# Kernel tuning notes

Hardware: AMD Instinct MI355X
Metric: run time of the kernel (lower is better)

## Reference

```python
import jax, jax.numpy as jnp
import numpy as np

EMB = 1024
HEADS = 16
HEADSIZE = EMB // HEADS
LN_EPS = 1e-5


def layernorm(x, w, b):
    # normalize over last dim (headsize)
    mu = jnp.mean(x, axis=-1, keepdims=True)
    var = jnp.var(x, axis=-1, keepdims=True)
    return (x - mu) * jax.lax.rsqrt(var + LN_EPS) * w + b


def setup_inputs() -> dict:
    key = jax.random.key(0)
    ks = jax.random.split(key, 8)
    B, S, C = 2, 2048, 2048
    x = jax.random.normal(ks[0], (B, S, EMB), dtype=jnp.float32)
    context = jax.random.normal(ks[1], (B, C, EMB), dtype=jnp.float32)
    mask = jnp.ones((B, S), dtype=jnp.float32)
    contextMask = jnp.ones((B, C), dtype=jnp.float32)
    s = 0.02
    Wq = jax.random.normal(ks[2], (EMB, EMB), dtype=jnp.float32) * s
    Wk = jax.random.normal(ks[3], (EMB, EMB), dtype=jnp.float32) * s
    Wv = jax.random.normal(ks[4], (EMB, EMB), dtype=jnp.float32) * s
    Wu = jax.random.normal(ks[5], (EMB, EMB), dtype=jnp.float32) * s
    bu = jnp.zeros((EMB,), dtype=jnp.float32)
    qln_w = jnp.ones((HEADSIZE,), dtype=jnp.float32)
    qln_b = jnp.zeros((HEADSIZE,), dtype=jnp.float32)
    kln_w = jnp.ones((HEADSIZE,), dtype=jnp.float32)
    kln_b = jnp.zeros((HEADSIZE,), dtype=jnp.float32)
    return {"x": x, "context": context, "mask": mask, "contextMask": contextMask,
            "Wq": Wq, "Wk": Wk, "Wv": Wv, "Wu": Wu, "bu": bu,
            "qln_w": qln_w, "qln_b": qln_b, "kln_w": kln_w, "kln_b": kln_b}


def reference(x, context, mask, contextMask, Wq, Wk, Wv, Wu, bu, qln_w, qln_b, kln_w, kln_b):
    B, S, E = x.shape
    C = context.shape[1]
    T = S + C
    xc = jnp.concatenate([x, context], axis=1)            # [B, T, E]
    q = (x @ Wq).reshape(B, S, HEADS, HEADSIZE)
    k = (xc @ Wk).reshape(B, T, HEADS, HEADSIZE)
    v = (xc @ Wv).reshape(B, T, HEADS, HEADSIZE)
    q = layernorm(q, qln_w, qln_b)
    k = layernorm(k, kln_w, kln_b)
    scale = E ** 0.25
    q = q / scale
    k = k / scale
    # [B, H, S, T] score matrix (explicitly materialized, as in the original)
    dot = jnp.einsum('bshd,bthd->bhst', q, k)
    mcat = jnp.concatenate([mask, contextMask], axis=1)   # [B, T]
    dotMask = mask[:, None, :, None] * mcat[:, None, None, :]  # [B,1,S,T]
    # hand-rolled masked softmax: softmax(dot*mask) * mask, renormalize
    p = jax.nn.softmax(dot * dotMask, axis=-1) * dotMask
    p = p / (jnp.sum(p, axis=-1, keepdims=True) + 1e-13)
    out = jnp.einsum('bhst,bthd->bshd', p, v).reshape(B, S, E)
    return out @ Wu + bu
```

## Files before the change

kernel.cpp:

```cpp
#include <hip/hip_runtime.h>
#include <hip/hip_bf16.h>
#include <cstdint>

#define B_SZ   2
#define S_LEN  2048
#define C_LEN  2048
#define T_LEN  4096
#define EMB_   1024
#define HEADS_ 16
#define D_     64

typedef __attribute__((ext_vector_type(8))) short bf16x8;
typedef __attribute__((ext_vector_type(4))) float f32x4;
typedef __attribute__((ext_vector_type(16))) float f32x16;
typedef __attribute__((ext_vector_type(2))) float f32x2;

__device__ __forceinline__ unsigned short f2bf(float f) {
    unsigned u = __builtin_bit_cast(unsigned, f);
    u += 0x7fffu + ((u >> 16) & 1u);
    return (unsigned short)(u >> 16);
}
__device__ __forceinline__ float bf2f(unsigned short h) {
    return __builtin_bit_cast(float, (unsigned)h << 16);
}

__global__ void build_xcb_k(const float* __restrict__ x, const float* __restrict__ ctx,
                            unsigned short* __restrict__ xcb) {
    int i = blockIdx.x * blockDim.x + threadIdx.x;
    size_t e8 = (size_t)i * 8;
    int b = (int)(e8 / ((size_t)T_LEN * EMB_));
    size_t rem = e8 % ((size_t)T_LEN * EMB_);
    int t = (int)(rem / EMB_);
    int c = (int)(rem % EMB_);
    const float* src = (t < S_LEN)
        ? &x[((size_t)b * S_LEN + t) * EMB_ + c]
        : &ctx[((size_t)b * C_LEN + (t - S_LEN)) * EMB_ + c];
    float4 v0 = ((const float4*)src)[0];
    float4 v1 = ((const float4*)src)[1];
    uint4 o;
    o.x = (unsigned)f2bf(v0.x) | ((unsigned)f2bf(v0.y) << 16);
    o.y = (unsigned)f2bf(v0.z) | ((unsigned)f2bf(v0.w) << 16);
    o.z = (unsigned)f2bf(v1.x) | ((unsigned)f2bf(v1.y) << 16);
    o.w = (unsigned)f2bf(v1.z) | ((unsigned)f2bf(v1.w) << 16);
    *(uint4*)&xcb[e8] = o;
}

__global__ void mcat_k(const float* __restrict__ mask, const float* __restrict__ cmask,
                       float* __restrict__ Mcat) {
    int i = blockIdx.x * 256 + threadIdx.x;
    int b = i / T_LEN, t = i % T_LEN;
    Mcat[i] = (t < S_LEN) ? mask[(size_t)b * S_LEN + t]
                          : cmask[(size_t)b * C_LEN + (t - S_LEN)];
}

__global__ void wtrans4_k(const float* __restrict__ W0, const float* __restrict__ W1,
                          const float* __restrict__ W2, const float* __restrict__ W3,
                          unsigned short* __restrict__ T0, unsigned short* __restrict__ T1,
                          unsigned short* __restrict__ T2, unsigned short* __restrict__ T3) {
    __shared__ __align__(16) unsigned short tile[64][72];
    int bx = blockIdx.x, by = blockIdx.y, bz = blockIdx.z;
    const float* W = (bz == 0) ? W0 : (bz == 1) ? W1 : (bz == 2) ? W2 : W3;
    unsigned short* WT = (bz == 0) ? T0 : (bz == 1) ? T1 : (bz == 2) ? T2 : T3;
    int tid = threadIdx.x;
#pragma unroll
    for (int r = 0; r < 4; ++r) {
        int idx = tid + r * 256;
        int row = idx >> 4, c4 = idx & 15;
        float4 v = ((const float4*)&W[((size_t)(by * 64 + row)) * EMB_ + bx * 64])[c4];
        tile[row][c4 * 4 + 0] = f2bf(v.x);
        tile[row][c4 * 4 + 1] = f2bf(v.y);
        tile[row][c4 * 4 + 2] = f2bf(v.z);
        tile[row][c4 * 4 + 3] = f2bf(v.w);
    }
    __syncthreads();
#pragma unroll
    for (int r = 0; r < 2; ++r) {
        int idx = tid + r * 256;
        int n = idx >> 3, k8 = idx & 7;
        uint4 o;
        unsigned q[4];
#pragma unroll
        for (int j = 0; j < 4; ++j)
            q[j] = (unsigned)tile[k8 * 8 + 2 * j][n] | ((unsigned)tile[k8 * 8 + 2 * j + 1][n] << 16);
        o.x = q[0]; o.y = q[1]; o.z = q[2]; o.w = q[3];
        *(uint4*)&WT[((size_t)(bx * 64 + n)) * EMB_ + by * 64 + k8 * 8] = o;
    }
}

__global__ __launch_bounds__(256) void gemm_qkv_k(
    const unsigned short* __restrict__ A,
    const unsigned short* __restrict__ Bt,
    unsigned short* __restrict__ Yk,
    unsigned short* __restrict__ Yv,
    unsigned short* __restrict__ Yq) {
    constexpr int KTOT = 1024, NTOT = 1024;
    int nt = blockIdx.x, mt = blockIdx.y;
    if (nt >= 16 && (mt & 31) >= 16) return;
    __shared__ __align__(16) unsigned short As[128 * 32];
    __shared__ __align__(16) unsigned short Bs[128 * 32];
    int in_row0 = mt * 128;
    unsigned short* Cout;
    int col0, out_row0;
    if (nt < 8)       { Cout = Yk; col0 = nt * 128;        out_row0 = mt * 128; }
    else if (nt < 16) { Cout = Yv; col0 = (nt - 8) * 128;  out_row0 = mt * 128; }
    else              { Cout = Yq; col0 = (nt - 16) * 128;
                        out_row0 = (mt >> 5) * 2048 + (mt & 31) * 128; }
    int tid = threadIdx.x, w = tid >> 6, l = tid & 63, l15 = l & 15, lg = l >> 4;
    int wr = (w >> 1) * 64, wc = (w & 1) * 64;

    f32x4 zero4 = {0.f, 0.f, 0.f, 0.f};
    f32x4 acc[4][4];
#pragma unroll
    for (int i = 0; i < 4; ++i)
#pragma unroll
        for (int j = 0; j < 4; ++j) acc[i][j] = zero4;

    for (int k0 = 0; k0 < KTOT; k0 += 32) {
#pragma unroll
        for (int j = 0; j < 2; ++j) {
            int o = tid * 16 + j * 4096;
            int row = o >> 6;
            int ke = (o & 63) >> 1;
            __builtin_amdgcn_global_load_lds(
                (const __attribute__((address_space(1))) void*)&A[(size_t)(in_row0 + row) * KTOT + k0 + ke],
                (__attribute__((address_space(3))) void*)&As[o >> 1], 16, 0, 0);
            __builtin_amdgcn_global_load_lds(
                (const __attribute__((address_space(1))) void*)&Bt[(size_t)(nt * 128 + row) * KTOT + k0 + ke],
                (__attribute__((address_space(3))) void*)&Bs[o >> 1], 16, 0, 0);
        }
        __syncthreads();
        bf16x8 af[4], bf[4];
#pragma unroll
        for (int fr = 0; fr < 4; ++fr)
            af[fr] = *(const bf16x8*)&As[(wr + fr * 16 + l15) * 32 + lg * 8];
#pragma unroll
        for (int fc = 0; fc < 4; ++fc)
            bf[fc] = *(const bf16x8*)&Bs[(wc + fc * 16 + l15) * 32 + lg * 8];
#pragma unroll
        for (int fr = 0; fr < 4; ++fr)
#pragma unroll
            for (int fc = 0; fc < 4; ++fc)
                acc[fr][fc] = __builtin_amdgcn_mfma_f32_16x16x32_bf16(af[fr], bf[fc], acc[fr][fc], 0, 0, 0);
        __syncthreads();
    }
#pragma unroll
    for (int fr = 0; fr < 4; ++fr) {
#pragma unroll
        for (int fc = 0; fc < 4; ++fc) {
            int row = out_row0 + wr + fr * 16 + lg * 4;
            int col = col0 + wc + fc * 16 + l15;
#pragma unroll
            for (int i = 0; i < 4; ++i)
                Cout[(size_t)(row + i) * NTOT + col] = f2bf(acc[fr][fc][i]);
        }
    }
}

template <bool F32OUT>
__global__ __launch_bounds__(256) void gemm_bt_k(
    const unsigned short* __restrict__ A,
    const unsigned short* __restrict__ Bt,
    void* __restrict__ Cout,
    const float* __restrict__ bias,
    int mtiles_per_chunk, int chunk_stride) {
    constexpr int KTOT = 1024, NTOT = 1024;
    __shared__ __align__(16) unsigned short As[128 * 32];
    __shared__ __align__(16) unsigned short Bs[128 * 32];
    int nt = blockIdx.x, mt = blockIdx.y;
    int in_row0 = (mt / mtiles_per_chunk) * chunk_stride + (mt % mtiles_per_chunk) * 128;
    int out_row0 = mt * 128;
    int tid = threadIdx.x, w = tid >> 6, l = tid & 63, l15 = l & 15, lg = l >> 4;
    int wr = (w >> 1) * 64, wc = (w & 1) * 64;

    f32x4 zero4 = {0.f, 0.f, 0.f, 0.f};
    f32x4 acc[4][4];
#pragma unroll
    for (int i = 0; i < 4; ++i)
#pragma unroll
        for (int j = 0; j < 4; ++j) acc[i][j] = zero4;

    for (int k0 = 0; k0 < KTOT; k0 += 32) {
#pragma unroll
        for (int j = 0; j < 2; ++j) {
            int o = tid * 16 + j * 4096;
            int row = o >> 6;
            int ke = (o & 63) >> 1;
            __builtin_amdgcn_global_load_lds(
                (const __attribute__((address_space(1))) void*)&A[(size_t)(in_row0 + row) * KTOT + k0 + ke],
                (__attribute__((address_space(3))) void*)&As[o >> 1], 16, 0, 0);
            __builtin_amdgcn_global_load_lds(
                (const __attribute__((address_space(1))) void*)&Bt[(size_t)(nt * 128 + row) * KTOT + k0 + ke],
                (__attribute__((address_space(3))) void*)&Bs[o >> 1], 16, 0, 0);
        }
        __syncthreads();
        bf16x8 af[4], bf[4];
#pragma unroll
        for (int fr = 0; fr < 4; ++fr)
            af[fr] = *(const bf16x8*)&As[(wr + fr * 16 + l15) * 32 + lg * 8];
#pragma unroll
        for (int fc = 0; fc < 4; ++fc)
            bf[fc] = *(const bf16x8*)&Bs[(wc + fc * 16 + l15) * 32 + lg * 8];
#pragma unroll
        for (int fr = 0; fr < 4; ++fr)
#pragma unroll
            for (int fc = 0; fc < 4; ++fc)
                acc[fr][fc] = __builtin_amdgcn_mfma_f32_16x16x32_bf16(af[fr], bf[fc], acc[fr][fc], 0, 0, 0);
        __syncthreads();
    }
#pragma unroll
    for (int fr = 0; fr < 4; ++fr) {
#pragma unroll
        for (int fc = 0; fc < 4; ++fc) {
            int row = out_row0 + wr + fr * 16 + lg * 4;
            int col = nt * 128 + wc + fc * 16 + l15;
#pragma unroll
            for (int i = 0; i < 4; ++i) {
                float v = acc[fr][fc][i];
                if (F32OUT) {
                    ((float*)Cout)[(size_t)(row + i) * NTOT + col] = v + bias[col];
                } else {
                    ((unsigned short*)Cout)[(size_t)(row + i) * NTOT + col] = f2bf(v);
                }
            }
        }
    }
}

__global__ void ln_head_k(const unsigned short* __restrict__ Y,
                          unsigned short* __restrict__ Out,
                          const float* __restrict__ lw, const float* __restrict__ lb,
                          const float* __restrict__ Mcat,
                          int rows_per_b, float scale) {
    int gw = blockIdx.x * 4 + (threadIdx.x >> 6);
    int lane = threadIdx.x & 63;
    int h = gw % HEADS_;
    int row = gw / HEADS_;
    int b = row / rows_per_b, r = row % rows_per_b;
    float v = bf2f(Y[(size_t)row * EMB_ + h * 64 + lane]);
    float s = v, s2 = v * v;
#pragma unroll
    for (int m = 1; m <= 32; m <<= 1) {
        s += __shfl_xor(s, m);
        s2 += __shfl_xor(s2, m);
    }
    float mu = s * (1.f / 64.f);
    float var = s2 * (1.f / 64.f) - mu * mu;
    float o = (v - mu) * rsqrtf(var + 1e-5f) * lw[lane] + lb[lane];
    float mq = Mcat[(size_t)b * T_LEN + r];
    Out[(((size_t)b * HEADS_ + h) * rows_per_b + r) * 64 + lane] = f2bf(o * scale * mq);
}

__global__ void ln_head_pack_k(const unsigned short* __restrict__ Y,
                               unsigned short* __restrict__ KF,
                               const float* __restrict__ lw, const float* __restrict__ lb,
                               const float* __restrict__ Mcat,
                               float scale) {
    int gw = blockIdx.x * 4 + (threadIdx.x >> 6);
    int lane = threadIdx.x & 63;
    int h = gw % HEADS_;
    int row = gw / HEADS_;
    int b = row / T_LEN, r = row % T_LEN;
    float v = bf2f(Y[(size_t)row * EMB_ + h * 64 + lane]);
    float s = v, s2 = v * v;
#pragma unroll
    for (int m = 1; m <= 32; m <<= 1) {
        s += __shfl_xor(s, m);
        s2 += __shfl_xor(s2, m);
    }
    float mu = s * (1.f / 64.f);
    float var = s2 * (1.f / 64.f) - mu * mu;
    float o = (v - mu) * rsqrtf(var + 1e-5f) * lw[lane] + lb[lane];
    float mt = Mcat[(size_t)b * T_LEN + r];
    int bh = b * HEADS_ + h;
    int kt = r >> 5, l31 = r & 31;
    int sf = lane >> 4, hi = (lane >> 3) & 1, j = lane & 7;
    size_t flat = ((((size_t)bh * 128 + kt) * 4 + sf) * 64 + hi * 32 + l31) * 8 + j;
    KF[flat] = f2bf(o * scale * mt);
}

__global__ void vpack_k(const unsigned short* __restrict__ Yv, unsigned short* __restrict__ VF,
                        const float* __restrict__ Mcat) {
    __shared__ __align__(16) unsigned short tile[64][72];
    __shared__ float msk[64];
    int t0 = blockIdx.x * 64;
    int bh = blockIdx.y;
    int b = bh >> 4, h = bh & 15;
    int tid = threadIdx.x;
    if (tid < 64) msk[tid] = Mcat[(size_t)b * T_LEN + t0 + tid];
#pragma unroll
    for (int rr = 0; rr < 2; ++rr) {
        int idx = tid + rr * 256;
        int row = idx >> 3, c8 = idx & 7;
        *(uint4*)&tile[row][c8 * 8] =
            *(const uint4*)&Yv[((size_t)b * T_LEN + t0 + row) * EMB_ + h * 64 + c8 * 8];
    }
    __syncthreads();
    int f = tid >> 6, l = tid & 63;
    int d = (f >> 1) * 32 + (l & 31);
    int tb = (f & 1) * 16 + 4 * (l >> 5);
#pragma unroll
    for (int ktl = 0; ktl < 2; ++ktl) {
        unsigned short e[8];
#pragma unroll
        for (int j = 0; j < 8; ++j) {
            int tt = ktl * 32 + tb + (j >> 2) * 8 + (j & 3);
            e[j] = f2bf(bf2f(tile[tt][d]) * msk[tt]);
        }
        uint4 o;
        o.x = (unsigned)e[0] | ((unsigned)e[1] << 16);
        o.y = (unsigned)e[2] | ((unsigned)e[3] << 16);
        o.z = (unsigned)e[4] | ((unsigned)e[5] << 16);
        o.w = (unsigned)e[6] | ((unsigned)e[7] << 16);
        size_t kt = (size_t)blockIdx.x * 2 + ktl;
        *(uint4*)&VF[((((size_t)bh * 128 + kt) * 4 + f) * 64 + l) * 8] = o;
    }
}

#define SOFTMAX(SA, MT, LS, PB0, PB1) do {                                        \
    f32x2 e2[8];                                                                  \
    _Pragma("unroll") for (int i_ = 0; i_ < 8; ++i_) {                            \
        e2[i_][0] = __builtin_amdgcn_exp2f(SA[2 * i_]);                           \
        e2[i_][1] = __builtin_amdgcn_exp2f(SA[2 * i_ + 1]);                       \
    }                                                                             \
    {                                                                             \
        float rsA_ = 0.f, rsB_ = 0.f;                                             \
        _Pragma("unroll") for (int i_ = 0; i_ < 8; ++i_) {                        \
            rsA_ = fmaf(e2[i_][0], MT[2 * i_], rsA_);                             \
            rsB_ = fmaf(e2[i_][1], MT[2 * i_ + 1], rsB_);                         \
        }                                                                         \
        float rs_ = rsA_ + rsB_;                                                  \
        rs_ += __shfl_xor(rs_, 32);                                               \
        (LS) += rs_;                                                              \
    }                                                                             \
    unsigned pk_[8];                                                              \
    _Pragma("unroll") for (int d_ = 0; d_ < 8; ++d_)                              \
        asm("v_cvt_pk_bf16_f32 %0, %1, %2" : "=v"(pk_[d_])                        \
            : "v"(e2[d_][0]), "v"(e2[d_][1]));                                    \
    { uint4 u0_; u0_.x=pk_[0]; u0_.y=pk_[1]; u0_.z=pk_[2]; u0_.w=pk_[3];          \
      uint4 u1_; u1_.x=pk_[4]; u1_.y=pk_[5]; u1_.z=pk_[6]; u1_.w=pk_[7];          \
      (PB0) = __builtin_bit_cast(bf16x8, u0_);                                    \
      (PB1) = __builtin_bit_cast(bf16x8, u1_); }                                  \
} while (0)

__global__ __launch_bounds__(256) void attn32_k(
    const unsigned short* __restrict__ Q,
    const unsigned short* __restrict__ KF,
    const unsigned short* __restrict__ VF,
    const float* __restrict__ Mcat,
    unsigned short* __restrict__ O) {
    __shared__ __align__(16) unsigned short Ks[4][2048];
    __shared__ __align__(16) unsigned short Vs[4][2048];
    __shared__ float OldsF[4][64][32];
    __shared__ float Llds[4][32];

    int bid = blockIdx.x;
    int xcd = bid & 7, slot = bid >> 3;
    int bh = xcd * 4 + (slot >> 4);
    int qblk = slot & 15;
    int b = bh >> 4, h = bh & 15;
    int tid = threadIdx.x;
    int w = tid >> 6;
    int lane = tid & 63;
    int l31 = lane & 31;
    int hi = lane >> 5;
    int q0 = qblk * 128;
    int qw = q0 + w * 32;

    const unsigned short* KFb_ = KF + (size_t)bh * 262144;
    const unsigned short* VFb_ = VF + (size_t)bh * 262144;
    const float* Mb = Mcat + (size_t)b * T_LEN;

    bf16x8 qf[4];
    {
        const unsigned short* Qp = Q + ((size_t)bh * S_LEN + qw + l31) * 64 + hi * 8;
#pragma unroll
        for (int s = 0; s < 4; ++s) qf[s] = *(const bf16x8*)(Qp + s * 16);
    }

    f32x16 Z16;
#pragma unroll
    for (int i = 0; i < 16; ++i) Z16[i] = 0.f;
    f32x16 acc0 = Z16, acc1 = Z16;
    float lS = 0.f;

#define STAGE(BUF, KT) do {                                                        \
    __builtin_amdgcn_global_load_lds(                                              \
        (const __attribute__((address_space(1))) void*)(KFb_ + (size_t)(KT) * 2048 + tid * 8), \
        (__attribute__((address_space(3))) void*)&Ks[BUF][tid * 8], 16, 0, 0);     \
    __builtin_amdgcn_global_load_lds(                                              \
        (const __attribute__((address_space(1))) void*)(VFb_ + (size_t)(KT) * 2048 + tid * 8), \
        (__attribute__((address_space(3))) void*)&Vs[BUF][tid * 8], 16, 0, 0);     \
} while (0)

    STAGE(0, 0); STAGE(1, 1);
    __syncthreads();

    for (int it = 0; it < 64; ++it) {
        int base = (it & 1) << 1;
        int kt0 = it * 2;
        if (it < 63) {
            STAGE(base ^ 2, kt0 + 2);
            STAGE((base ^ 2) + 1, kt0 + 3);
        }
        const float* mb0 = Mb + kt0 * 32 + 4 * hi;
        float4 am0 = *(const float4*)(mb0);
        float4 am1 = *(const float4*)(mb0 + 8);
        float4 am2 = *(const float4*)(mb0 + 16);
        float4 am3 = *(const float4*)(mb0 + 24);
        float4 bm0 = *(const float4*)(mb0 + 32);
        float4 bm1 = *(const float4*)(mb0 + 40);
        float4 bm2 = *(const float4*)(mb0 + 48);
        float4 bm3 = *(const float4*)(mb0 + 56);
        bf16x8 kfrA[4], vfrA[4], kfrB[4], vfrB[4];
#pragma unroll
        for (int s = 0; s < 4; ++s) {
            kfrA[s] = *(const bf16x8*)&Ks[base][s * 512 + lane * 8];
            vfrA[s] = *(const bf16x8*)&Vs[base][s * 512 + lane * 8];
            kfrB[s] = *(const bf16x8*)&Ks[base + 1][s * 512 + lane * 8];
            vfrB[s] = *(const bf16x8*)&Vs[base + 1][s * 512 + lane * 8];
        }
        f32x16 saA = Z16, saB = Z16;
#pragma unroll
        for (int s = 0; s < 4; ++s) {
            saA = __builtin_amdgcn_mfma_f32_32x32x16_bf16(kfrA[s], qf[s], saA, 0, 0, 0);
            saB = __builtin_amdgcn_mfma_f32_32x32x16_bf16(kfrB[s], qf[s], saB, 0, 0, 0);
        }
        float mtA_[16], mtB_[16];
        mtA_[0] = am0.x; mtA_[1] = am0.y; mtA_[2]  = am0.z; mtA_[3]  = am0.w;
        mtA_[4] = am1.x; mtA_[5] = am1.y; mtA_[6]  = am1.z; mtA_[7]  = am1.w;
        mtA_[8] = am2.x; mtA_[9] = am2.y; mtA_[10] = am2.z; mtA_[11] = am2.w;
        mtA_[12] = am3.x; mtA_[13] = am3.y; mtA_[14] = am3.z; mtA_[15] = am3.w;
        mtB_[0] = bm0.x; mtB_[1] = bm0.y; mtB_[2]  = bm0.z; mtB_[3]  = bm0.w;
        mtB_[4] = bm1.x; mtB_[5] = bm1.y; mtB_[6]  = bm1.z; mtB_[7]  = bm1.w;
        mtB_[8] = bm2.x; mtB_[9] = bm2.y; mtB_[10] = bm2.z; mtB_[11] = bm2.w;
        mtB_[12] = bm3.x; mtB_[13] = bm3.y; mtB_[14] = bm3.z; mtB_[15] = bm3.w;
        bf16x8 p0A, p1A, p0B, p1B;
        SOFTMAX(saA, mtA_, lS, p0A, p1A);
        SOFTMAX(saB, mtB_, lS, p0B, p1B);
        acc0 = __builtin_amdgcn_mfma_f32_32x32x16_bf16(vfrA[0], p0A, acc0, 0, 0, 0);
        acc1 = __builtin_amdgcn_mfma_f32_32x32x16_bf16(vfrA[2], p0A, acc1, 0, 0, 0);
        acc0 = __builtin_amdgcn_mfma_f32_32x32x16_bf16(vfrA[1], p1A, acc0, 0, 0, 0);
        acc1 = __builtin_amdgcn_mfma_f32_32x32x16_bf16(vfrA[3], p1A, acc1, 0, 0, 0);
        acc0 = __builtin_amdgcn_mfma_f32_32x32x16_bf16(vfrB[0], p0B, acc0, 0, 0, 0);
        acc1 = __builtin_amdgcn_mfma_f32_32x32x16_bf16(vfrB[2], p0B, acc1, 0, 0, 0);
        acc0 = __builtin_amdgcn_mfma_f32_32x32x16_bf16(vfrB[1], p1B, acc0, 0, 0, 0);
        acc1 = __builtin_amdgcn_mfma_f32_32x32x16_bf16(vfrB[3], p1B, acc1, 0, 0, 0);
        __syncthreads();
    }
#undef STAGE

#pragma unroll
    for (int r = 0; r < 16; ++r) {
        int dl = (r & 3) + 8 * (r >> 2) + 4 * hi;
        OldsF[w][dl][l31] = acc0[r];
        OldsF[w][dl + 32][l31] = acc1[r];
    }
    if (hi == 0) Llds[w][l31] = lS;
    __syncthreads();
    {
        int rr = lane >> 1, hf = lane & 1;
        float L = Llds[w][rr];
        float invL = 1.f / (L + 1e-13f);
        float mqz = Mb[q0 + w * 32 + rr];
        invL = (mqz != 0.f) ? invL : 0.f;
        float v_[32];
#pragma unroll
        for (int dd = 0; dd < 32; ++dd)
            v_[dd] = OldsF[w][hf * 32 + dd][rr] * invL;
        unsigned po_[16];
#pragma unroll
        for (int d2 = 0; d2 < 16; ++d2)
            asm("v_cvt_pk_bf16_f32 %0, %1, %2" : "=v"(po_[d2]) : "v"(v_[2*d2]), "v"(v_[2*d2+1]));
        unsigned short* Orow = &O[((size_t)b * S_LEN + qw + rr) * EMB_ + h * 64 + hf * 32];
#pragma unroll
        for (int i = 0; i < 4; ++i) {
            uint4 st;
            st.x = po_[4*i]; st.y = po_[4*i+1]; st.z = po_[4*i+2]; st.w = po_[4*i+3];
            *(uint4*)(Orow + i * 8) = st;
        }
    }
}

extern "C" void kernel_launch(void* const* d_in, const int* in_sizes, int n_in,
                              void* d_out, int out_size, void* d_ws, size_t ws_size,
                              hipStream_t stream) {
    const float* x     = (const float*)d_in[0];
    const float* ctx   = (const float*)d_in[1];
    const float* mask  = (const float*)d_in[2];
    const float* cmask = (const float*)d_in[3];
    const float* Wq    = (const float*)d_in[4];
    const float* Wk    = (const float*)d_in[5];
    const float* Wv    = (const float*)d_in[6];
    const float* Wu    = (const float*)d_in[7];
    const float* bu    = (const float*)d_in[8];
    const float* qlnw  = (const float*)d_in[9];
    const float* qlnb  = (const float*)d_in[10];
    const float* klnw  = (const float*)d_in[11];
    const float* klnb  = (const float*)d_in[12];

    unsigned short* ws = (unsigned short*)d_ws;
    unsigned short* xcb = ws + 0;
    unsigned short* WkT = ws + 8388608;
    unsigned short* WvT = ws + 9437184;
    unsigned short* WqT = ws + 10485760;
    unsigned short* Qb  = ws + 0;
    unsigned short* KFb = ws + 4194304;
    unsigned short* WuT = ws + 12582912;
    unsigned short* Yq  = ws + 13631488;
    unsigned short* Ob  = Yq;
    unsigned short* Yk  = ws + 17825792;
    unsigned short* VFb = Yk;
    unsigned short* Yv  = ws + 26214400;
    float* Mcat         = (float*)(ws + 34603008);

    const float scale = 0.17677669529663687f;
    const float qscale = 0.17677669529663687f * 1.4426950408889634f;

    build_xcb_k<<<4096, 256, 0, stream>>>(x, ctx, xcb);
    mcat_k<<<32, 256, 0, stream>>>(mask, cmask, Mcat);
    wtrans4_k<<<dim3(16, 16, 4), 256, 0, stream>>>(Wk, Wv, Wq, Wu, WkT, WvT, WqT, WuT);

    gemm_qkv_k<<<dim3(24, 64), 256, 0, stream>>>(xcb, WkT, Yk, Yv, Yq);

    ln_head_k<<<16384, 256, 0, stream>>>(Yq, Qb, qlnw, qlnb, Mcat, S_LEN, qscale);
    ln_head_pack_k<<<32768, 256, 0, stream>>>(Yk, KFb, klnw, klnb, Mcat, scale);
    vpack_k<<<dim3(64, 32), 256, 0, stream>>>(Yv, VFb, Mcat);

    attn32_k<<<512, 256, 0, stream>>>(Qb, KFb, VFb, Mcat, Ob);

    gemm_bt_k<true><<<dim3(8, 32), 256, 0, stream>>>(Ob, WuT, d_out, bu, 32, 4096);
}
```

Before: 239.1 us.

## Fuse head LayerNorm, masking and K/V packing into QKV GEMM epilogue

Moves the per-head LayerNorm for Q and K, the mask scaling, and the K/V fragment packing into the epilogue of the QKV projection GEMM. Each warp's 64-column tile covers exactly one head, so the row statistics come from register sums plus a 16-lane shuffle. This removes three separate kernels and the round trip of the intermediate Yq/Yk/Yv buffers through global memory. The cost is scattered 2-byte stores in the packed layouts, which may coalesce poorly, plus extra register pressure in the GEMM epilogue.

```diff
diff --git a/kernel.cpp b/kernel.cpp
--- a/kernel.cpp
+++ b/kernel.cpp
@@ -87,24 +87,24 @@
     }
 }
 
-__global__ __launch_bounds__(256) void gemm_qkv_k(
+__global__ __launch_bounds__(256) void gemm_qkv_fused_k(
     const unsigned short* __restrict__ A,
     const unsigned short* __restrict__ Bt,
-    unsigned short* __restrict__ Yk,
-    unsigned short* __restrict__ Yv,
-    unsigned short* __restrict__ Yq) {
-    constexpr int KTOT = 1024, NTOT = 1024;
+    unsigned short* __restrict__ KF,
+    unsigned short* __restrict__ VF,
+    unsigned short* __restrict__ Qb,
+    const float* __restrict__ qlnw, const float* __restrict__ qlnb,
+    const float* __restrict__ klnw, const float* __restrict__ klnb,
+    const float* __restrict__ Mcat,
+    float kscale, float qscale) {
+    constexpr int KTOT = 1024;
     int nt = blockIdx.x, mt = blockIdx.y;
     if (nt >= 16 && (mt & 31) >= 16) return;
     __shared__ __align__(16) unsigned short As[128 * 32];
     __shared__ __align__(16) unsigned short Bs[128 * 32];
     int in_row0 = mt * 128;
-    unsigned short* Cout;
-    int col0, out_row0;
-    if (nt < 8)       { Cout = Yk; col0 = nt * 128;        out_row0 = mt * 128; }
-    else if (nt < 16) { Cout = Yv; col0 = (nt - 8) * 128;  out_row0 = mt * 128; }
-    else              { Cout = Yq; col0 = (nt - 16) * 128;
-                        out_row0 = (mt >> 5) * 2048 + (mt & 31) * 128; }
+    int mode = (nt < 8) ? 0 : (nt < 16) ? 1 : 2;
+    int col0 = (mode == 0) ? nt * 128 : (mode == 1) ? (nt - 8) * 128 : (nt - 16) * 128;
     int tid = threadIdx.x, w = tid >> 6, l = tid & 63, l15 = l & 15, lg = l >> 4;
     int wr = (w >> 1) * 64, wc = (w & 1) * 64;
 
@@ -143,15 +143,74 @@
                 acc[fr][fc] = __builtin_amdgcn_mfma_f32_16x16x32_bf16(af[fr], bf[fc], acc[fr][fc], 0, 0, 0);
         __syncthreads();
     }
+
+    int h = (col0 + wc) >> 6;
+    float lwv[4], lbv[4];
+    if (mode == 0) {
+#pragma unroll
+        for (int fc = 0; fc < 4; ++fc) { lwv[fc] = klnw[fc * 16 + l15]; lbv[fc] = klnb[fc * 16 + l15]; }
+    } else if (mode == 2) {
+#pragma unroll
+        for (int fc = 0; fc < 4; ++fc) { lwv[fc] = qlnw[fc * 16 + l15]; lbv[fc] = qlnb[fc * 16 + l15]; }
+    }
 #pragma unroll
     for (int fr = 0; fr < 4; ++fr) {
 #pragma unroll
-        for (int fc = 0; fc < 4; ++fc) {
-            int row = out_row0 + wr + fr * 16 + lg * 4;
-            int col = col0 + wc + fc * 16 + l15;
-#pragma unroll
-            for (int i = 0; i < 4; ++i)
-                Cout[(size_t)(row + i) * NTOT + col] = f2bf(acc[fr][fc][i]);
+        for (int i = 0; i < 4; ++i) {
+            float mu = 0.f, rstd = 0.f;
+            if (mode != 1) {
+                float s  = acc[fr][0][i] + acc[fr][1][i] + acc[fr][2][i] + acc[fr][3][i];
+                float s2 = acc[fr][0][i] * acc[fr][0][i] + acc[fr][1][i] * acc[fr][1][i]
+                         + acc[fr][2][i] * acc[fr][2][i] + acc[fr][3][i] * acc[fr][3][i];
+#pragma unroll
+                for (int m = 1; m <= 8; m <<= 1) {
+                    s  += __shfl_xor(s, m);
+                    s2 += __shfl_xor(s2, m);
+                }
+                mu = s * (1.f / 64.f);
+                float var = s2 * (1.f / 64.f) - mu * mu;
+                rstd = rsqrtf(var + 1e-5f);
+            }
+            if (mode == 2) {
+                int r = (mt & 31) * 128 + wr + fr * 16 + lg * 4 + i;
+                int bq = mt >> 5;
+                float mq = Mcat[(size_t)bq * T_LEN + r];
+                size_t bh = (size_t)(bq * HEADS_ + h);
+#pragma unroll
+                for (int fc = 0; fc < 4; ++fc) {
+                    int dh = fc * 16 + l15;
+                    float o = (acc[fr][fc][i] - mu) * rstd * lwv[fc] + lbv[fc];
+                    Qb[(bh * S_LEN + r) * 64 + dh] = f2bf(o * qscale * mq);
+                }
+            } else {
+                int grow = in_row0 + wr + fr * 16 + lg * 4 + i;
+                int bb = grow >> 12, t = grow & 4095;
+                float mt_ = Mcat[(size_t)bb * T_LEN + t];
+                size_t bh = (size_t)(bb * HEADS_ + h);
+                int kt = t >> 5, t31 = t & 31;
+                if (mode == 0) {
+#pragma unroll
+                    for (int fc = 0; fc < 4; ++fc) {
+                        int dh = fc * 16 + l15;
+                        float o = (acc[fr][fc][i] - mu) * rstd * lwv[fc] + lbv[fc];
+                        size_t flat = (((bh * 128 + kt) * 4 + (dh >> 4)) * 64
+                                       + ((dh >> 3) & 1) * 32 + t31) * 8 + (dh & 7);
+                        KF[flat] = f2bf(o * kscale * mt_);
+                    }
+                } else {
+                    int f1 = (t31 >> 4) & 1;
+                    int j = ((t31 >> 3) & 1) * 4 + (t31 & 3);
+                    int lofs = ((t31 >> 2) & 1) * 32;
+#pragma unroll
+                    for (int fc = 0; fc < 4; ++fc) {
+                        int dh = fc * 16 + l15;
+                        int f = (dh >> 5) * 2 + f1;
+                        int ll = lofs + (dh & 31);
+                        size_t flat = (((bh * 128 + kt) * 4 + f) * 64 + ll) * 8 + j;
+                        VF[flat] = f2bf(acc[fr][fc][i] * mt_);
+                    }
+                }
+            }
         }
     }
 }
@@ -223,96 +282,6 @@
                 }
             }
         }
-    }
-}
-
-__global__ void ln_head_k(const unsigned short* __restrict__ Y,
-                          unsigned short* __restrict__ Out,
-                          const float* __restrict__ lw, const float* __restrict__ lb,
-                          const float* __restrict__ Mcat,
-                          int rows_per_b, float scale) {
-    int gw = blockIdx.x * 4 + (threadIdx.x >> 6);
-    int lane = threadIdx.x & 63;
-    int h = gw % HEADS_;
-    int row = gw / HEADS_;
-    int b = row / rows_per_b, r = row % rows_per_b;
-    float v = bf2f(Y[(size_t)row * EMB_ + h * 64 + lane]);
-    float s = v, s2 = v * v;
-#pragma unroll
-    for (int m = 1; m <= 32; m <<= 1) {
-        s += __shfl_xor(s, m);
-        s2 += __shfl_xor(s2, m);
-    }
-    float mu = s * (1.f / 64.f);
-    float var = s2 * (1.f / 64.f) - mu * mu;
-    float o = (v - mu) * rsqrtf(var + 1e-5f) * lw[lane] + lb[lane];
-    float mq = Mcat[(size_t)b * T_LEN + r];
-    Out[(((size_t)b * HEADS_ + h) * rows_per_b + r) * 64 + lane] = f2bf(o * scale * mq);
-}
-
-__global__ void ln_head_pack_k(const unsigned short* __restrict__ Y,
-                               unsigned short* __restrict__ KF,
-                               const float* __restrict__ lw, const float* __restrict__ lb,
-                               const float* __restrict__ Mcat,
-                               float scale) {
-    int gw = blockIdx.x * 4 + (threadIdx.x >> 6);
-    int lane = threadIdx.x & 63;
-    int h = gw % HEADS_;
-    int row = gw / HEADS_;
-    int b = row / T_LEN, r = row % T_LEN;
-    float v = bf2f(Y[(size_t)row * EMB_ + h * 64 + lane]);
-    float s = v, s2 = v * v;
-#pragma unroll
-    for (int m = 1; m <= 32; m <<= 1) {
-        s += __shfl_xor(s, m);
-        s2 += __shfl_xor(s2, m);
-    }
-    float mu = s * (1.f / 64.f);
-    float var = s2 * (1.f / 64.f) - mu * mu;
-    float o = (v - mu) * rsqrtf(var + 1e-5f) * lw[lane] + lb[lane];
-    float mt = Mcat[(size_t)b * T_LEN + r];
-    int bh = b * HEADS_ + h;
-    int kt = r >> 5, l31 = r & 31;
-    int sf = lane >> 4, hi = (lane >> 3) & 1, j = lane & 7;
-    size_t flat = ((((size_t)bh * 128 + kt) * 4 + sf) * 64 + hi * 32 + l31) * 8 + j;
-    KF[flat] = f2bf(o * scale * mt);
-}
-
-__global__ void vpack_k(const unsigned short* __restrict__ Yv, unsigned short* __restrict__ VF,
-                        const float* __restrict__ Mcat) {
-    __shared__ __align__(16) unsigned short tile[64][72];
-    __shared__ float msk[64];
-    int t0 = blockIdx.x * 64;
-    int bh = blockIdx.y;
-    int b = bh >> 4, h = bh & 15;
-    int tid = threadIdx.x;
-    if (tid < 64) msk[tid] = Mcat[(size_t)b * T_LEN + t0 + tid];
-#pragma unroll
-    for (int rr = 0; rr < 2; ++rr) {
-        int idx = tid + rr * 256;
-        int row = idx >> 3, c8 = idx & 7;
-        *(uint4*)&tile[row][c8 * 8] =
-            *(const uint4*)&Yv[((size_t)b * T_LEN + t0 + row) * EMB_ + h * 64 + c8 * 8];
-    }
-    __syncthreads();
-    int f = tid >> 6, l = tid & 63;
-    int d = (f >> 1) * 32 + (l & 31);
-    int tb = (f & 1) * 16 + 4 * (l >> 5);
-#pragma unroll
-    for (int ktl = 0; ktl < 2; ++ktl) {
-        unsigned short e[8];
-#pragma unroll
-        for (int j = 0; j < 8; ++j) {
-            int tt = ktl * 32 + tb + (j >> 2) * 8 + (j & 3);
-            e[j] = f2bf(bf2f(tile[tt][d]) * msk[tt]);
-        }
-        uint4 o;
-        o.x = (unsigned)e[0] | ((unsigned)e[1] << 16);
-        o.y = (unsigned)e[2] | ((unsigned)e[3] << 16);
-        o.z = (unsigned)e[4] | ((unsigned)e[5] << 16);
-        o.w = (unsigned)e[6] | ((unsigned)e[7] << 16);
-        size_t kt = (size_t)blockIdx.x * 2 + ktl;
-        *(uint4*)&VF[((((size_t)bh * 128 + kt) * 4 + f) * 64 + l) * 8] = o;
     }
 }
 
@@ -503,14 +472,11 @@
     unsigned short* WkT = ws + 8388608;
     unsigned short* WvT = ws + 9437184;
     unsigned short* WqT = ws + 10485760;
-    unsigned short* Qb  = ws + 0;
-    unsigned short* KFb = ws + 4194304;
     unsigned short* WuT = ws + 12582912;
-    unsigned short* Yq  = ws + 13631488;
-    unsigned short* Ob  = Yq;
-    unsigned short* Yk  = ws + 17825792;
-    unsigned short* VFb = Yk;
-    unsigned short* Yv  = ws + 26214400;
+    unsigned short* Qb  = ws + 13631488;
+    unsigned short* KFb = ws + 17825792;
+    unsigned short* VFb = ws + 26214400;
+    unsigned short* Ob  = ws + 0;
     float* Mcat         = (float*)(ws + 34603008);
 
     const float scale = 0.17677669529663687f;
@@ -520,11 +486,8 @@
     mcat_k<<<32, 256, 0, stream>>>(mask, cmask, Mcat);
     wtrans4_k<<<dim3(16, 16, 4), 256, 0, stream>>>(Wk, Wv, Wq, Wu, WkT, WvT, WqT, WuT);
 
-    gemm_qkv_k<<<dim3(24, 64), 256, 0, stream>>>(xcb, WkT, Yk, Yv, Yq);
-
-    ln_head_k<<<16384, 256, 0, stream>>>(Yq, Qb, qlnw, qlnb, Mcat, S_LEN, qscale);
-    ln_head_pack_k<<<32768, 256, 0, stream>>>(Yk, KFb, klnw, klnb, Mcat, scale);
-    vpack_k<<<dim3(64, 32), 256, 0, stream>>>(Yv, VFb, Mcat);
+    gemm_qkv_fused_k<<<dim3(24, 64), 256, 0, stream>>>(
+        xcb, WkT, KFb, VFb, Qb, qlnw, qlnb, klnw, klnb, Mcat, scale, qscale);
 
     attn32_k<<<512, 256, 0, stream>>>(Qb, KFb, VFb, Mcat, Ob);
 
```

Result: faster. 230.5 us (-3.6%).
